# Performance work log

Hardware: AMD Instinct MI355X
Metric: run time of the kernel (lower is better)

Reference implementation:

```python
import jax, jax.numpy as jnp
import numpy as np

B, S, H = 4, 512, 768
D, M = 24, 96          # hdim_proj_dim, hdim_mlp_hidden
O = 2 * max(128, H // 2)  # val_mlp hidden = 768


def setup_inputs() -> dict:
    key = jax.random.key(0)
    ks = jax.random.split(key, 14)
    u = lambda k, shp, fan_in: jax.random.uniform(k, shp, jnp.float32, -1.0, 1.0) / np.float32(np.sqrt(fan_in))
    return {
        'H_j': jax.random.normal(ks[0], (B, S, H), jnp.float32),
        'H_i': jax.random.normal(ks[1], (B, S, H), jnp.float32),
        'Wpj': u(ks[2], (H, D), H),
        'Wpi': u(ks[3], (H, D), H),
        'Ws1': u(ks[4], (4 * D, M), 4 * D),
        'bs1': u(ks[5], (M,), 4 * D),
        'ws2': u(ks[6], (M,), M),
        'bs2': u(ks[7], (), M),
        'Wv1': u(ks[8], (3 * H, O), 3 * H),
        'bv1': u(ks[9], (O,), 3 * H),
        'Wv2': u(ks[10], (O, H), O),
        'bv2': u(ks[11], (H,), O),
        'alpha': jnp.float32(0.05),
        'attn_mask': jnp.ones((B, S), jnp.int32),
    }


def reference(H_j, H_i, Wpj, Wpi, Ws1, bs1, ws2, bs2, Wv1, bv1, Wv2, bv2, alpha, attn_mask):
    # Projections [B,S,D]
    Zj = H_j @ Wpj
    Zi = H_i @ Wpi
    # 4term score MLP, first layer decomposed over the concat blocks:
    # cat(Zj_p, Zi_p, Zj_p*Zi_p, |Zj_p - Zi_p|) @ Ws1
    W1j, W1i, W1h, W1d = Ws1[:D], Ws1[D:2 * D], Ws1[2 * D:3 * D], Ws1[3 * D:]
    tj = Zj @ W1j                                   # [B,P,M]
    ti = Zi @ W1i                                   # [B,Q,M]
    th = jnp.einsum('bpd,bqd,dm->bpqm', Zj, Zi, W1h)  # hadamard term
    diff = jnp.abs(Zj[:, :, None, :] - Zi[:, None, :, :])  # [B,P,Q,D]
    td = jnp.einsum('bpqd,dm->bpqm', diff, W1d)
    hid = jax.nn.relu(tj[:, :, None, :] + ti[:, None, :, :] + th + td + bs1)  # [B,P,Q,M]
    logits = jnp.einsum('bpqm,m->bpq', hid, ws2) + bs2  # [B,P,Q]
    # mask over source tokens (last dim); token_temp == 1.0 so no division
    mask = attn_mask.astype(logits.dtype)
    logits = logits + (1.0 - mask)[:, None, :] * jnp.finfo(logits.dtype).min
    probs = jax.nn.softmax(logits, axis=-1)
    ctx = jnp.einsum('bpq,bqh->bph', probs, H_i)    # [B,S,H]
    # val_mlp on cat(ctx, H_j, ctx*H_j), first layer decomposed
    Wc, Wj, Wh = Wv1[:H], Wv1[H:2 * H], Wv1[2 * H:]
    mhid = jax.nn.relu(ctx @ Wc + H_j @ Wj + (ctx * H_j) @ Wh + bv1)
    msg = mhid @ Wv2 + bv2
    # dropout is identity in eval mode
    return alpha * msg
```

## Files before the change

kernel.cpp:

```cpp
#include <hip/hip_runtime.h>
#include <hip/hip_bf16.h>

#define Bb 4
#define Ss 512
#define Hh 768
#define Dd 24
#define Mm 96
#define Oo 768

typedef __bf16 bf16x8 __attribute__((ext_vector_type(8)));
typedef float f32x4 __attribute__((ext_vector_type(4)));

__device__ __forceinline__ void transpose_tile(
    const float* __restrict__ s, __bf16* __restrict__ d,
    int R, int C, int bx, int by, float* smem, int tid)
{
    const int x = tid & 31, y = tid >> 5;
    const int c0 = bx * 32, r0 = by * 32;
    #pragma unroll
    for (int i = 0; i < 4; ++i)
        smem[(y + 8 * i) * 33 + x] = s[(size_t)(r0 + y + 8 * i) * C + c0 + x];
    __syncthreads();
    #pragma unroll
    for (int i = 0; i < 4; ++i)
        d[(size_t)(c0 + y + 8 * i) * R + r0 + x] = (__bf16)smem[x * 33 + (y + 8 * i)];
}

__global__ __launch_bounds__(256) void prep_kernel(
    const float* __restrict__ Hj, const float* __restrict__ Hi,
    const float* __restrict__ Wpj, const float* __restrict__ Wpi,
    const float* __restrict__ Wv1, const float* __restrict__ Wv2,
    float* __restrict__ Zj, float* __restrict__ Zi,
    __bf16* __restrict__ HiT, __bf16* __restrict__ Wv1T,
    __bf16* __restrict__ Wv2T, __bf16* __restrict__ Acat)
{
    __shared__ float smem[1088];
    const int bid = blockIdx.x;
    const int tid = threadIdx.x;

    if (bid < 4096) {
        const int row = bid & 2047;
        const int which = bid >> 11;
        const float* src = (which ? Hi : Hj) + (size_t)row * Hh;
        const float* W = which ? Wpi : Wpj;
        float* Z = which ? Zi : Zj;
        float* rowbuf = smem;
        float* partial = smem + 768;
        for (int i = tid; i < Hh; i += 256) rowbuf[i] = src[i];
        __syncthreads();
        if (tid < 192) {
            const int d = tid % Dd;
            const int c = tid / Dd;
            const int h0 = c * 96;
            float s = 0.f;
            #pragma unroll 4
            for (int h = h0; h < h0 + 96; ++h) s = fmaf(rowbuf[h], W[h * Dd + d], s);
            partial[c * Dd + d] = s;
        }
        __syncthreads();
        if (tid < Dd) {
            float s = 0.f;
            #pragma unroll
            for (int c = 0; c < 8; ++c) s += partial[c * Dd + tid];
            Z[(size_t)row * Dd + tid] = s;
        }
    } else if (bid < 5632) {
        int rem = bid - 4096;
        const int bz = rem / 384; rem %= 384;
        transpose_tile(Hi + (size_t)bz * Ss * Hh, HiT + (size_t)bz * Hh * Ss,
                       Ss, Hh, rem % 24, rem / 24, smem, tid);
    } else if (bid < 7360) {
        const int rem = bid - 5632;
        transpose_tile(Wv1, Wv1T, 3 * Hh, Oo, rem % 24, rem / 24, smem, tid);
    } else if (bid < 7936) {
        const int rem = bid - 7360;
        transpose_tile(Wv2, Wv2T, Oo, Hh, rem % 24, rem / 24, smem, tid);
    } else {
        const int idx = (bid - 7936) * 256 + tid;
        const int row = idx / 96, c8 = idx % 96;
        const float* s = Hj + (size_t)row * Hh + c8 * 8;
        const float4 u = *(const float4*)s;
        const float4 v = *(const float4*)(s + 4);
        bf16x8 o;
        o[0]=(__bf16)u.x; o[1]=(__bf16)u.y; o[2]=(__bf16)u.z; o[3]=(__bf16)u.w;
        o[4]=(__bf16)v.x; o[5]=(__bf16)v.y; o[6]=(__bf16)v.z; o[7]=(__bf16)v.w;
        *(bf16x8*)&Acat[(size_t)row * 2304 + Hh + c8 * 8] = o;
    }
}

__global__ __launch_bounds__(256) void pair_kernel(
    const float* __restrict__ Zj, const float* __restrict__ Zi,
    const float* __restrict__ Ws1, const float* __restrict__ bs1,
    const float* __restrict__ ws2, const float* __restrict__ bs2p,
    const int* __restrict__ mask, __bf16* __restrict__ probs)
{
    const int bp = blockIdx.x;
    const int b  = bp >> 9;
    const int tid  = threadIdx.x;
    const int lane = tid & 63;
    const int wid  = tid >> 6;
    const int col  = lane & 15;
    const int g    = lane >> 4;

    __shared__ float zjall[Dd];
    __shared__ float rowadd[Mm];
    __shared__ float logitsl[Ss];
    __shared__ float red[8];

    if (tid < Dd) zjall[tid] = Zj[(size_t)bp * Dd + tid];
    __syncthreads();
    if (tid < Mm) {
        float s = bs1[tid];
        #pragma unroll
        for (int d = 0; d < Dd; ++d) s = fmaf(zjall[d], Ws1[d * Mm + tid], s);
        rowadd[tid] = s;
    }
    __syncthreads();

    float zj8[8];
    if (g < 3) {
        const float* zr = Zj + (size_t)bp * Dd + g * 8;
        const float4 u = *(const float4*)zr;
        const float4 v = *(const float4*)(zr + 4);
        zj8[0]=u.x; zj8[1]=u.y; zj8[2]=u.z; zj8[3]=u.w;
        zj8[4]=v.x; zj8[5]=v.y; zj8[6]=v.z; zj8[7]=v.w;
    } else {
        #pragma unroll
        for (int j = 0; j < 8; ++j) zj8[j] = 0.f;
    }

    bf16x8 bw[6][2];
    float ws2r[6];
    #pragma unroll
    for (int n = 0; n < 6; ++n) {
        const int m = n * 16 + col;
        ws2r[n] = ws2[m];
        bf16x8 b0, b1;
        if (g < 3) {
            #pragma unroll
            for (int j = 0; j < 8; ++j) {
                const int d = g * 8 + j;
                b0[j] = (__bf16)(fmaf(zj8[j], Ws1[(2 * Dd + d) * Mm + m],
                                      Ws1[(Dd + d) * Mm + m]));
                b1[j] = (__bf16)(Ws1[(3 * Dd + d) * Mm + m]);
            }
        } else {
            #pragma unroll
            for (int j = 0; j < 8; ++j) { b0[j] = (__bf16)0.f; b1[j] = (__bf16)0.f; }
            b0[0] = (__bf16)rowadd[m];
        }
        bw[n][0] = b0; bw[n][1] = b1;
    }

    const float* zib = Zi + (size_t)b * Ss * Dd;

    #pragma unroll 2
    for (int t = 0; t < 8; ++t) {
        const int q0 = wid * 128 + t * 16;
        bf16x8 a0, a1;
        if (g < 3) {
            const float* zr = zib + (size_t)(q0 + col) * Dd + g * 8;
            const float4 u = *(const float4*)zr;
            const float4 v = *(const float4*)(zr + 4);
            a0[0]=(__bf16)u.x; a0[1]=(__bf16)u.y; a0[2]=(__bf16)u.z; a0[3]=(__bf16)u.w;
            a0[4]=(__bf16)v.x; a0[5]=(__bf16)v.y; a0[6]=(__bf16)v.z; a0[7]=(__bf16)v.w;
            a1[0]=(__bf16)fabsf(zj8[0]-u.x); a1[1]=(__bf16)fabsf(zj8[1]-u.y);
            a1[2]=(__bf16)fabsf(zj8[2]-u.z); a1[3]=(__bf16)fabsf(zj8[3]-u.w);
            a1[4]=(__bf16)fabsf(zj8[4]-v.x); a1[5]=(__bf16)fabsf(zj8[5]-v.y);
            a1[6]=(__bf16)fabsf(zj8[6]-v.z); a1[7]=(__bf16)fabsf(zj8[7]-v.w);
        } else {
            #pragma unroll
            for (int j = 0; j < 8; ++j) { a0[j] = (__bf16)0.f; a1[j] = (__bf16)0.f; }
            a0[0] = (__bf16)1.0f;
        }

        f32x4 acc[6];
        #pragma unroll
        for (int n = 0; n < 6; ++n) acc[n] = (f32x4){0.f, 0.f, 0.f, 0.f};
        #pragma unroll
        for (int n = 0; n < 6; ++n) {
            acc[n] = __builtin_amdgcn_mfma_f32_16x16x32_bf16(a0, bw[n][0], acc[n], 0, 0, 0);
            acc[n] = __builtin_amdgcn_mfma_f32_16x16x32_bf16(a1, bw[n][1], acc[n], 0, 0, 0);
        }

        float lsum[4] = {0.f, 0.f, 0.f, 0.f};
        #pragma unroll
        for (int n = 0; n < 6; ++n)
            #pragma unroll
            for (int r = 0; r < 4; ++r)
                lsum[r] = fmaf(fmaxf(acc[n][r], 0.f), ws2r[n], lsum[r]);
        #pragma unroll
        for (int off = 1; off <= 8; off <<= 1) {
            #pragma unroll
            for (int r = 0; r < 4; ++r) lsum[r] += __shfl_xor(lsum[r], off);
        }
        if (col == 0) {
            float4 o = {lsum[0], lsum[1], lsum[2], lsum[3]};
            *(float4*)&logitsl[q0 + g * 4] = o;
        }
    }
    __syncthreads();

    const float bs2v = bs2p[0];
    const int* mrow = mask + (size_t)b * Ss;
    float l0 = logitsl[tid]       + bs2v + (1.0f - (float)mrow[tid])       * (-3.402823466e+38f);
    float l1 = logitsl[tid + 256] + bs2v + (1.0f - (float)mrow[tid + 256]) * (-3.402823466e+38f);
    float vmax = fmaxf(l0, l1);
    #pragma unroll
    for (int off = 32; off > 0; off >>= 1) vmax = fmaxf(vmax, __shfl_xor(vmax, off));
    if (lane == 0) red[wid] = vmax;
    __syncthreads();
    const float mx = fmaxf(fmaxf(red[0], red[1]), fmaxf(red[2], red[3]));
    const float e0 = __expf(l0 - mx);
    const float e1 = __expf(l1 - mx);
    float vs = e0 + e1;
    #pragma unroll
    for (int off = 32; off > 0; off >>= 1) vs += __shfl_xor(vs, off);
    if (lane == 0) red[4 + wid] = vs;
    __syncthreads();
    const float inv = 1.0f / (red[4] + red[5] + red[6] + red[7]);
    __bf16* prow = probs + (size_t)bp * Ss;
    prow[tid] = (__bf16)(e0 * inv);
    prow[tid + 256] = (__bf16)(e1 * inv);
}

template<int MODE>
__global__ __launch_bounds__(256) void gemm_kernel(
    const __bf16* __restrict__ A, const __bf16* __restrict__ Bt,
    const float* __restrict__ Hjf, const float* __restrict__ bias,
    const float* __restrict__ alphap,
    __bf16* __restrict__ obf, float* __restrict__ of)
{
    constexpr int K = (MODE == 0) ? 512 : (MODE == 1) ? 2304 : 768;
    constexpr int NIT = K / 64;
    constexpr int LDT = 72;

    __shared__ __bf16 As[64 * LDT];
    __shared__ __bf16 Bs[64 * LDT];

    const int tid = threadIdx.x;
    const int lane = tid & 63;
    const int wid = tid >> 6;
    const int col = lane & 15, g = lane >> 4;
    const int wm = wid >> 1, wn = wid & 1;
    const int r0 = blockIdx.x * 64;
    const int n0 = blockIdx.y * 64;
    const __bf16* Btb = (MODE == 0) ? Bt + (size_t)(r0 >> 9) * (Hh * Ss) : Bt;

    const int srow = tid >> 2;
    const int sc8  = (tid & 3) * 16;
    const __bf16* ag = A   + (size_t)(r0 + srow) * K + sc8;
    const __bf16* bg = Btb + (size_t)(n0 + srow) * K + sc8;
    __bf16* asl = &As[srow * LDT + sc8];
    __bf16* bsl = &Bs[srow * LDT + sc8];

    bf16x8 ra0 = *(const bf16x8*)(ag);
    bf16x8 ra1 = *(const bf16x8*)(ag + 8);
    bf16x8 rb0 = *(const bf16x8*)(bg);
    bf16x8 rb1 = *(const bf16x8*)(bg + 8);

    f32x4 acc[2][2];
    #pragma unroll
    for (int mi = 0; mi < 2; ++mi)
        #pragma unroll
        for (int ni = 0; ni < 2; ++ni) acc[mi][ni] = (f32x4){0.f, 0.f, 0.f, 0.f};

    for (int it = 0; it < NIT; ++it) {
        __syncthreads();
        *(bf16x8*)(asl)     = ra0;
        *(bf16x8*)(asl + 8) = ra1;
        *(bf16x8*)(bsl)     = rb0;
        *(bf16x8*)(bsl + 8) = rb1;
        __syncthreads();
        if (it + 1 < NIT) {
            const int kk = (it + 1) * 64;
            ra0 = *(const bf16x8*)(ag + kk);
            ra1 = *(const bf16x8*)(ag + kk + 8);
            rb0 = *(const bf16x8*)(bg + kk);
            rb1 = *(const bf16x8*)(bg + kk + 8);
        }
        #pragma unroll
        for (int h = 0; h < 2; ++h) {
            bf16x8 a0 = *(const bf16x8*)&As[(wm * 32 + col)      * LDT + h * 32 + g * 8];
            bf16x8 a1 = *(const bf16x8*)&As[(wm * 32 + 16 + col) * LDT + h * 32 + g * 8];
            bf16x8 b0 = *(const bf16x8*)&Bs[(wn * 32 + col)      * LDT + h * 32 + g * 8];
            bf16x8 b1 = *(const bf16x8*)&Bs[(wn * 32 + 16 + col) * LDT + h * 32 + g * 8];
            acc[0][0] = __builtin_amdgcn_mfma_f32_16x16x32_bf16(a0, b0, acc[0][0], 0, 0, 0);
            acc[0][1] = __builtin_amdgcn_mfma_f32_16x16x32_bf16(a0, b1, acc[0][1], 0, 0, 0);
            acc[1][0] = __builtin_amdgcn_mfma_f32_16x16x32_bf16(a1, b0, acc[1][0], 0, 0, 0);
            acc[1][1] = __builtin_amdgcn_mfma_f32_16x16x32_bf16(a1, b1, acc[1][1], 0, 0, 0);
        }
    }

    const float al = (MODE == 2) ? alphap[0] : 0.f;
    #pragma unroll
    for (int mi = 0; mi < 2; ++mi) {
        #pragma unroll
        for (int r = 0; r < 4; ++r) {
            const int row = r0 + wm * 32 + mi * 16 + g * 4 + r;
            #pragma unroll
            for (int ni = 0; ni < 2; ++ni) {
                const int cn = n0 + wn * 32 + ni * 16 + col;
                const float v = acc[mi][ni][r];
                if (MODE == 0) {
                    const float hjv = Hjf[(size_t)row * Hh + cn];
                    obf[(size_t)row * 2304 + cn] = (__bf16)v;
                    obf[(size_t)row * 2304 + 1536 + cn] = (__bf16)(v * hjv);
                } else if (MODE == 1) {
                    obf[(size_t)row * Oo + cn] = (__bf16)fmaxf(v + bias[cn], 0.f);
                } else {
                    of[(size_t)row * Hh + cn] = al * (v + bias[cn]);
                }
            }
        }
    }
}

extern "C" void kernel_launch(void* const* d_in, const int* in_sizes, int n_in,
                              void* d_out, int out_size, void* d_ws, size_t ws_size,
                              hipStream_t stream)
{
    const float* Hj  = (const float*)d_in[0];
    const float* Hi  = (const float*)d_in[1];
    const float* Wpj = (const float*)d_in[2];
    const float* Wpi = (const float*)d_in[3];
    const float* Ws1 = (const float*)d_in[4];
    const float* bs1 = (const float*)d_in[5];
    const float* ws2 = (const float*)d_in[6];
    const float* bs2 = (const float*)d_in[7];
    const float* Wv1 = (const float*)d_in[8];
    const float* bv1 = (const float*)d_in[9];
    const float* Wv2 = (const float*)d_in[10];
    const float* bv2 = (const float*)d_in[11];
    const float* alpha = (const float*)d_in[12];
    const int* mask  = (const int*)d_in[13];

    float* ws = (float*)d_ws;
    float* Zj      = ws;
    float* Zi      = Zj + 49152;
    float* probs_f = Zi + 49152;
    float* HiT_f   = probs_f + 524288;
    float* Wv2T_f  = HiT_f + 786432;
    float* mhid_f  = Wv2T_f + 294912;
    float* Acat_f  = mhid_f + 786432;
    float* Wv1T_f  = Acat_f + 2359296;

    __bf16* probs_bf = (__bf16*)probs_f;
    __bf16* HiT      = (__bf16*)HiT_f;
    __bf16* Wv2T     = (__bf16*)Wv2T_f;
    __bf16* mhid_bf  = (__bf16*)mhid_f;
    __bf16* Acat     = (__bf16*)Acat_f;
    __bf16* Wv1T     = (__bf16*)Wv1T_f;

    prep_kernel<<<dim3(8704), 256, 0, stream>>>(
        Hj, Hi, Wpj, Wpi, Wv1, Wv2, Zj, Zi, HiT, Wv1T, Wv2T, Acat);
    pair_kernel<<<dim3(Bb * Ss), 256, 0, stream>>>(
        Zj, Zi, Ws1, bs1, ws2, bs2, mask, probs_bf);
    gemm_kernel<0><<<dim3(2048 / 64, Hh / 64), 256, 0, stream>>>(
        probs_bf, HiT, Hj, nullptr, nullptr, Acat, nullptr);
    gemm_kernel<1><<<dim3(2048 / 64, Oo / 64), 256, 0, stream>>>(
        Acat, Wv1T, nullptr, bv1, nullptr, mhid_bf, nullptr);
    gemm_kernel<2><<<dim3(2048 / 64, Hh / 64), 256, 0, stream>>>(
        mhid_bf, Wv2T, nullptr, bv2, alpha, nullptr, (float*)d_out);
}
```

Measured before the change: 183.5 us.

## Pipeline GEMM tiles via direct global-to-LDS loads with triple buffering and swizzle

The three bf16 GEMM kernels now load tiles straight into LDS with global_load_lds, use a three-stage ring buffer with explicit vmcnt waits and a single barrier per iteration, and apply an XOR swizzle in place of padding to avoid bank conflicts. The N tile grows from 64 to 96, so each wave computes a 32x48 output per step. The aim is to overlap global loads with MFMA work and cut register staging and sync overhead. The cost is a smaller grid (8 column tiles instead of 12) and reliance on hand-written waitcnt counts being correct.

```diff
diff --git a/kernel.cpp b/kernel.cpp
--- a/kernel.cpp
+++ b/kernel.cpp
@@ -224,6 +224,18 @@
     prow[tid + 256] = (__bf16)(e1 * inv);
 }
 
+__device__ __forceinline__ void gload16(const __bf16* g, __bf16* l)
+{
+    __builtin_amdgcn_global_load_lds(
+        (const __attribute__((address_space(1))) void*)g,
+        (__attribute__((address_space(3))) void*)l, 16, 0, 0);
+}
+
+__device__ __forceinline__ int swz(int row, int k)
+{
+    return row * 64 + (k ^ ((row & 7) << 3));
+}
+
 template<int MODE>
 __global__ __launch_bounds__(256) void gemm_kernel(
     const __bf16* __restrict__ A, const __bf16* __restrict__ Bt,
@@ -233,10 +245,9 @@
 {
     constexpr int K = (MODE == 0) ? 512 : (MODE == 1) ? 2304 : 768;
     constexpr int NIT = K / 64;
-    constexpr int LDT = 72;
-
-    __shared__ __bf16 As[64 * LDT];
-    __shared__ __bf16 Bs[64 * LDT];
+
+    __shared__ __align__(16) __bf16 As[3][64 * 64];
+    __shared__ __align__(16) __bf16 Bs[3][96 * 64];
 
     const int tid = threadIdx.x;
     const int lane = tid & 63;
@@ -244,51 +255,70 @@
     const int col = lane & 15, g = lane >> 4;
     const int wm = wid >> 1, wn = wid & 1;
     const int r0 = blockIdx.x * 64;
-    const int n0 = blockIdx.y * 64;
+    const int n0 = blockIdx.y * 96;
     const __bf16* Btb = (MODE == 0) ? Bt + (size_t)(r0 >> 9) * (Hh * Ss) : Bt;
 
-    const int srow = tid >> 2;
-    const int sc8  = (tid & 3) * 16;
-    const __bf16* ag = A   + (size_t)(r0 + srow) * K + sc8;
-    const __bf16* bg = Btb + (size_t)(n0 + srow) * K + sc8;
-    __bf16* asl = &As[srow * LDT + sc8];
-    __bf16* bsl = &Bs[srow * LDT + sc8];
-
-    bf16x8 ra0 = *(const bf16x8*)(ag);
-    bf16x8 ra1 = *(const bf16x8*)(ag + 8);
-    bf16x8 rb0 = *(const bf16x8*)(bg);
-    bf16x8 rb1 = *(const bf16x8*)(bg + 8);
-
-    f32x4 acc[2][2];
+    const __bf16* asrc[2];
+    const __bf16* bsrc[3];
+    int aldo[2], bldo[3];
+    #pragma unroll
+    for (int i = 0; i < 2; ++i) {
+        const int c = (wid * 2 + i) * 64 + lane;
+        const int row = c >> 3;
+        const int k16 = (c & 7) ^ (row & 7);
+        asrc[i] = A + (size_t)(r0 + row) * K + k16 * 8;
+        aldo[i] = (wid * 2 + i) * 512;
+    }
+    #pragma unroll
+    for (int i = 0; i < 3; ++i) {
+        const int c = (wid * 3 + i) * 64 + lane;
+        const int row = c >> 3;
+        const int k16 = (c & 7) ^ (row & 7);
+        bsrc[i] = Btb + (size_t)(n0 + row) * K + k16 * 8;
+        bldo[i] = (wid * 3 + i) * 512;
+    }
+
+    auto stage = [&](int t, int buf) {
+        __bf16* ab = &As[buf][0];
+        __bf16* bb = &Bs[buf][0];
+        #pragma unroll
+        for (int i = 0; i < 2; ++i) gload16(asrc[i] + (size_t)t * 64, ab + aldo[i]);
+        #pragma unroll
+        for (int i = 0; i < 3; ++i) gload16(bsrc[i] + (size_t)t * 64, bb + bldo[i]);
+    };
+
+    f32x4 acc[2][3];
     #pragma unroll
     for (int mi = 0; mi < 2; ++mi)
         #pragma unroll
-        for (int ni = 0; ni < 2; ++ni) acc[mi][ni] = (f32x4){0.f, 0.f, 0.f, 0.f};
+        for (int ni = 0; ni < 3; ++ni) acc[mi][ni] = (f32x4){0.f, 0.f, 0.f, 0.f};
+
+    stage(0, 0);
+    stage(1, 1);
 
     for (int it = 0; it < NIT; ++it) {
-        __syncthreads();
-        *(bf16x8*)(asl)     = ra0;
-        *(bf16x8*)(asl + 8) = ra1;
-        *(bf16x8*)(bsl)     = rb0;
-        *(bf16x8*)(bsl + 8) = rb1;
-        __syncthreads();
-        if (it + 1 < NIT) {
-            const int kk = (it + 1) * 64;
-            ra0 = *(const bf16x8*)(ag + kk);
-            ra1 = *(const bf16x8*)(ag + kk + 8);
-            rb0 = *(const bf16x8*)(bg + kk);
-            rb1 = *(const bf16x8*)(bg + kk + 8);
-        }
+        if (it < NIT - 1) asm volatile("s_waitcnt vmcnt(5)" ::: "memory");
+        else              asm volatile("s_waitcnt vmcnt(0)" ::: "memory");
+        __builtin_amdgcn_s_barrier();
+        __builtin_amdgcn_sched_barrier(0);
+        if (it + 2 < NIT) stage(it + 2, (it + 2) % 3);
+
+        const __bf16* Ac = As[it % 3];
+        const __bf16* Bc = Bs[it % 3];
         #pragma unroll
         for (int h = 0; h < 2; ++h) {
-            bf16x8 a0 = *(const bf16x8*)&As[(wm * 32 + col)      * LDT + h * 32 + g * 8];
-            bf16x8 a1 = *(const bf16x8*)&As[(wm * 32 + 16 + col) * LDT + h * 32 + g * 8];
-            bf16x8 b0 = *(const bf16x8*)&Bs[(wn * 32 + col)      * LDT + h * 32 + g * 8];
-            bf16x8 b1 = *(const bf16x8*)&Bs[(wn * 32 + 16 + col) * LDT + h * 32 + g * 8];
+            const int ka = h * 32 + g * 8;
+            const bf16x8 a0 = *(const bf16x8*)&Ac[swz(wm * 32 +      col, ka)];
+            const bf16x8 a1 = *(const bf16x8*)&Ac[swz(wm * 32 + 16 + col, ka)];
+            const bf16x8 b0 = *(const bf16x8*)&Bc[swz(wn * 48 +      col, ka)];
+            const bf16x8 b1 = *(const bf16x8*)&Bc[swz(wn * 48 + 16 + col, ka)];
+            const bf16x8 b2 = *(const bf16x8*)&Bc[swz(wn * 48 + 32 + col, ka)];
             acc[0][0] = __builtin_amdgcn_mfma_f32_16x16x32_bf16(a0, b0, acc[0][0], 0, 0, 0);
             acc[0][1] = __builtin_amdgcn_mfma_f32_16x16x32_bf16(a0, b1, acc[0][1], 0, 0, 0);
+            acc[0][2] = __builtin_amdgcn_mfma_f32_16x16x32_bf16(a0, b2, acc[0][2], 0, 0, 0);
             acc[1][0] = __builtin_amdgcn_mfma_f32_16x16x32_bf16(a1, b0, acc[1][0], 0, 0, 0);
             acc[1][1] = __builtin_amdgcn_mfma_f32_16x16x32_bf16(a1, b1, acc[1][1], 0, 0, 0);
+            acc[1][2] = __builtin_amdgcn_mfma_f32_16x16x32_bf16(a1, b2, acc[1][2], 0, 0, 0);
         }
     }
 
@@ -299,8 +329,8 @@
         for (int r = 0; r < 4; ++r) {
             const int row = r0 + wm * 32 + mi * 16 + g * 4 + r;
             #pragma unroll
-            for (int ni = 0; ni < 2; ++ni) {
-                const int cn = n0 + wn * 32 + ni * 16 + col;
+            for (int ni = 0; ni < 3; ++ni) {
+                const int cn = n0 + wn * 48 + ni * 16 + col;
                 const float v = acc[mi][ni][r];
                 if (MODE == 0) {
                     const float hjv = Hjf[(size_t)row * Hh + cn];
@@ -356,10 +386,10 @@
         Hj, Hi, Wpj, Wpi, Wv1, Wv2, Zj, Zi, HiT, Wv1T, Wv2T, Acat);
     pair_kernel<<<dim3(Bb * Ss), 256, 0, stream>>>(
         Zj, Zi, Ws1, bs1, ws2, bs2, mask, probs_bf);
-    gemm_kernel<0><<<dim3(2048 / 64, Hh / 64), 256, 0, stream>>>(
+    gemm_kernel<0><<<dim3(2048 / 64, Hh / 96), 256, 0, stream>>>(
         probs_bf, HiT, Hj, nullptr, nullptr, Acat, nullptr);
-    gemm_kernel<1><<<dim3(2048 / 64, Oo / 64), 256, 0, stream>>>(
+    gemm_kernel<1><<<dim3(2048 / 64, Oo / 96), 256, 0, stream>>>(
         Acat, Wv1T, nullptr, bv1, nullptr, mhid_bf, nullptr);
-    gemm_kernel<2><<<dim3(2048 / 64, Hh / 64), 256, 0, stream>>>(
+    gemm_kernel<2><<<dim3(2048 / 64, Hh / 96), 256, 0, stream>>>(
         mhid_bf, Wv2T, nullptr, bv2, alpha, nullptr, (float*)d_out);
 }
```

Measured after the change: 191.6 us. 1.04x slower.
